# Performance work log

Measured on AMD Instinct MI355X. Metric: run time of the kernel, lower is better.

The kernel has to match this reference:

```python
import jax, jax.numpy as jnp
import numpy as np

# ---- grid / spectral configuration (matches init_kwargs) ----
_LONS_HALF = [20 + 4 * i for i in range(1, 97)]
LONS = _LONS_HALF + _LONS_HALF[::-1]          # 192 rings, pole to pole
NLAT = len(LONS)                               # 192
TRUNC = 191
M = TRUNC + 1                                  # zonal wavenumbers kept
MAX_NLON = max(LONS)                           # 404
SLON = np.concatenate([[0], np.cumsum(LONS)[:-1]]).astype(np.int64)
NGRID = int(np.sum(LONS))                      # 41088
BATCH, CHAN = 16, 64
TWO_PI = 2.0 * np.pi


def _legpoly(mmax, lmax, x):
    """(-1)^m c^l_m P^l_m(x), shape (mmax+1, lmax+1, len(x)); same recurrences as source."""
    nmax = max(mmax, lmax)
    vdm = np.zeros((nmax + 1, nmax + 1, len(x)), dtype=np.float64)
    norm_factor = np.sqrt(4 * np.pi)  # forward transform (inverse=False)
    vdm[0, 0, :] = norm_factor / np.sqrt(4 * np.pi)
    for n in range(1, nmax + 1):
        vdm[n - 1, n, :] = np.sqrt(2 * n + 1) * x * vdm[n - 1, n - 1, :]
        vdm[n, n, :] = np.sqrt((2 * n + 1) * (1 + x) * (1 - x) / 2 / n) * vdm[n - 1, n - 1, :]
    for n in range(2, nmax + 1):
        for m in range(0, n - 1):
            vdm[m, n, :] = (x * np.sqrt((2 * n - 1) / (n - m) * (2 * n + 1) / (n + m)) * vdm[m, n - 1, :]
                            - np.sqrt((n + m - 1) / (n - m) * (2 * n + 1) / (2 * n - 3) * (n - m - 1) / (n + m)) * vdm[m, n - 2, :])
    return vdm[:mmax + 1, :lmax + 1]


def _build_buffers():
    # Legendre-Gauss nodes/weights on [-1, 1]
    xlg, wlg = np.polynomial.legendre.leggauss(NLAT)
    theta = np.flip(np.arccos(xlg))
    pct = _legpoly(TRUNC, TRUNC, np.cos(theta))          # (M, L, K)
    weight = (pct * wlg[None, None, :]).astype(np.float32)

    # Ragged per-ring real DFT expressed as masked cos/sin bases (== rfft, norm='forward')
    p = np.arange(MAX_NLON)
    m = np.arange(M)
    nlon = np.asarray(LONS, dtype=np.float64)[:, None, None]       # (K,1,1)
    ang = TWO_PI * m[None, None, :] * p[None, :, None] / nlon      # (K,P,M)
    valid = (p[None, :, None] < nlon) & (m[None, None, :] <= (np.asarray(LONS)[:, None, None] // 2))
    cos_basis = np.where(valid, np.cos(ang) / nlon, 0.0).astype(np.float32)
    sin_basis = np.where(valid, -np.sin(ang) / nlon, 0.0).astype(np.float32)

    # gather map: ring_idx[k, p] = SLON[k] + min(p, nlon_k - 1)  (clipped; basis masks the tail)
    ring_idx = (SLON[:, None] + np.minimum(p[None, :], np.asarray(LONS)[:, None] - 1)).astype(np.int32)
    return weight, cos_basis, sin_basis, ring_idx


def setup_inputs() -> dict:
    key = jax.random.key(0)
    x = jax.random.normal(key, (BATCH, CHAN, NGRID), dtype=jnp.float32)
    weight, cos_basis, sin_basis, ring_idx = _build_buffers()
    return {
        "x": x,
        "weight": jnp.asarray(weight),
        "cos_basis": jnp.asarray(cos_basis),
        "sin_basis": jnp.asarray(sin_basis),
        "ring_idx": jnp.asarray(ring_idx),
    }


def reference(x, weight, cos_basis, sin_basis, ring_idx):
    # gather grid points into padded rings: [..., K, P]
    xr = x[..., ring_idx]
    # per-ring rfft (norm='forward'), restricted to m <= TRUNC, scaled by 2*pi
    re = TWO_PI * jnp.einsum("bckp,kpm->bckm", xr, cos_basis)
    im = TWO_PI * jnp.einsum("bckp,kpm->bckm", xr, sin_basis)
    # weighted Legendre contraction over latitudes k: [..., l, m]
    rl = jnp.einsum("bckm,mlk->bclm", re, weight)
    il = jnp.einsum("bckm,mlk->bclm", im, weight)
    # real/imag stacked (== torch.view_as_real of the complex output)
    return jnp.stack((rl, il), axis=-1)
```

## Files before the change

### kernel.cpp

```cpp
#include <hip/hip_runtime.h>

#define NLAT 192
#define MM   192
#define LL   192
#define PMAX 404
#define NGRID 41088
#define BC   1024
#define TWO_PI_F 6.2831853071795864769f

__device__ __forceinline__ int kmin_of_m(int m) {
    return (m <= 12) ? 0 : ((m - 11) >> 1);
}

__global__ __launch_bounds__(256) void sht_stage1(
    const float* __restrict__ x,
    const float* __restrict__ cosb,
    const float* __restrict__ sinb,
    const int*   __restrict__ ring,
    float* __restrict__ ws,
    int bc0, int bcc)
{
    const int k   = blockIdx.z;
    const int m0  = blockIdx.y * 64;
    const int bct = blockIdx.x * 64;
    const int tid = threadIdx.x;
    const int tx  = tid & 15;
    const int ty  = tid >> 4;

    const int slon = ring[k * PMAX];
    const int nlon = ring[k * PMAX + PMAX - 1] - slon + 1;

    float* __restrict__ re_ws = ws;
    float* __restrict__ im_ws = ws + (size_t)MM * NLAT * bcc;

    if (m0 > (nlon >> 1)) {
        const int klo16 = kmin_of_m(m0) & ~15;
        if (k < klo16 || k > (NLAT - 1) - klo16) return;
        const float4 z = {0.f, 0.f, 0.f, 0.f};
#pragma unroll
        for (int j = 0; j < 4; ++j) {
            const int m = m0 + 4 * ty + j;
            const size_t base = ((size_t)m * NLAT + k) * bcc + bct + 4 * tx;
            *(float4*)&re_ws[base] = z;
            *(float4*)&im_ws[base] = z;
        }
        return;
    }

    __shared__ float xs[16][68];
    __shared__ float cs[16][64];
    __shared__ float ss[16][64];

    float accr[4][4] = {{0.f}};
    float acci[4][4] = {{0.f}};

    for (int p0 = 0; p0 < nlon; p0 += 16) {
        {
            const int pq = (tid & 3) * 4;
            const int bl = tid >> 2;
            float4 v = {0.f, 0.f, 0.f, 0.f};
            if (p0 + pq < nlon)
                v = *(const float4*)(x + (size_t)(bc0 + bct + bl) * NGRID + slon + p0 + pq);
            xs[pq + 0][bl] = v.x;
            xs[pq + 1][bl] = v.y;
            xs[pq + 2][bl] = v.z;
            xs[pq + 3][bl] = v.w;
        }
        {
            const int mq = (tid & 15) * 4;
            const int pl = tid >> 4;
            float4 c = {0.f, 0.f, 0.f, 0.f};
            float4 s = {0.f, 0.f, 0.f, 0.f};
            if (p0 + pl < PMAX) {
                const size_t off = ((size_t)k * PMAX + p0 + pl) * MM + m0 + mq;
                c = *(const float4*)(cosb + off);
                s = *(const float4*)(sinb + off);
            }
            *(float4*)&cs[pl][mq] = c;
            *(float4*)&ss[pl][mq] = s;
        }
        __syncthreads();

#pragma unroll
        for (int pp = 0; pp < 16; ++pp) {
            float xv[4], cv[4], sv[4];
            *(float4*)xv = *(const float4*)&xs[pp][4 * tx];
            *(float4*)cv = *(const float4*)&cs[pp][4 * ty];
            *(float4*)sv = *(const float4*)&ss[pp][4 * ty];
#pragma unroll
            for (int i = 0; i < 4; ++i)
#pragma unroll
                for (int j = 0; j < 4; ++j) {
                    accr[i][j] += xv[i] * cv[j];
                    acci[i][j] += xv[i] * sv[j];
                }
        }
        __syncthreads();
    }

#pragma unroll
    for (int j = 0; j < 4; ++j) {
        const int m = m0 + 4 * ty + j;
        const size_t base = ((size_t)m * NLAT + k) * bcc + bct + 4 * tx;
        float4 r = {accr[0][j] * TWO_PI_F, accr[1][j] * TWO_PI_F,
                    accr[2][j] * TWO_PI_F, accr[3][j] * TWO_PI_F};
        float4 s = {acci[0][j] * TWO_PI_F, acci[1][j] * TWO_PI_F,
                    acci[2][j] * TWO_PI_F, acci[3][j] * TWO_PI_F};
        *(float4*)&re_ws[base] = r;
        *(float4*)&im_ws[base] = s;
    }
}

__global__ __launch_bounds__(256) void sht_stage2(
    const float* __restrict__ ws,
    float* __restrict__ ws2,
    const float* __restrict__ weight,
    int bcc)
{
    const int m   = blockIdx.z;
    const int l0  = blockIdx.y * 64;
    const int bct = blockIdx.x * 128;
    if (l0 + 63 < m) return;

    const int tid = threadIdx.x;
    const int tx  = tid & 15;
    const int ty  = tid >> 4;

    const int klo16 = kmin_of_m(m) & ~15;
    const int pcnt  = 96 - klo16;

    const float* __restrict__ re_ws = ws;
    const float* __restrict__ im_ws = ws + (size_t)MM * NLAT * bcc;

    __shared__ float Ar[16][128];
    __shared__ float Br[16][128];
    __shared__ float Ai[16][128];
    __shared__ float Bi[16][128];
    __shared__ float wl[16][68];

    float accr[8][4] = {{0.f}};
    float acci[8][4] = {{0.f}};

    const bool modd = (m & 1) != 0;
    const int  srow = tid >> 5;
    const int  scol = (tid & 31) * 4;
    const int  wkk  = tid & 15;
    const int  wlw  = tid >> 4;

    for (int pc = 0; pc < pcnt; pc += 16) {
        const int p0 = klo16 + pc;
#pragma unroll
        for (int pass = 0; pass < 2; ++pass) {
            const int row = srow + pass * 8;
            const size_t offa = ((size_t)m * NLAT + (p0 + row)) * bcc + bct + scol;
            const size_t offb = ((size_t)m * NLAT + (191 - p0 - row)) * bcc + bct + scol;
            const float4 ar = *(const float4*)&re_ws[offa];
            const float4 br = *(const float4*)&re_ws[offb];
            const float4 ai = *(const float4*)&im_ws[offa];
            const float4 bi = *(const float4*)&im_ws[offb];
            float4 er = {ar.x + br.x, ar.y + br.y, ar.z + br.z, ar.w + br.w};
            float4 od = {ar.x - br.x, ar.y - br.y, ar.z - br.z, ar.w - br.w};
            float4 ei = {ai.x + bi.x, ai.y + bi.y, ai.z + bi.z, ai.w + bi.w};
            float4 oi = {ai.x - bi.x, ai.y - bi.y, ai.z - bi.z, ai.w - bi.w};
            if (modd) { float4 t = er; er = od; od = t; t = ei; ei = oi; oi = t; }
            *(float4*)&Ar[row][scol] = er;
            *(float4*)&Br[row][scol] = od;
            *(float4*)&Ai[row][scol] = ei;
            *(float4*)&Bi[row][scol] = oi;
        }
        {
#pragma unroll
            for (int r = 0; r < 4; ++r) {
                const int lc = wlw + r * 16;
                wl[wkk][lc] = weight[((size_t)m * LL + l0 + lc) * NLAT + p0 + wkk];
            }
        }
        __syncthreads();

#pragma unroll
        for (int kk = 0; kk < 16; ++kk) {
            const float4 ea = *(const float4*)&Ar[kk][4 * tx];
            const float4 eb = *(const float4*)&Ar[kk][64 + 4 * tx];
            const float4 oa = *(const float4*)&Br[kk][4 * tx];
            const float4 ob = *(const float4*)&Br[kk][64 + 4 * tx];
            const float4 fa = *(const float4*)&Ai[kk][4 * tx];
            const float4 fb = *(const float4*)&Ai[kk][64 + 4 * tx];
            const float4 ga = *(const float4*)&Bi[kk][4 * tx];
            const float4 gb = *(const float4*)&Bi[kk][64 + 4 * tx];
            const float4 wv = *(const float4*)&wl[kk][4 * ty];
            const float er8[8] = {ea.x, ea.y, ea.z, ea.w, eb.x, eb.y, eb.z, eb.w};
            const float or8[8] = {oa.x, oa.y, oa.z, oa.w, ob.x, ob.y, ob.z, ob.w};
            const float ei8[8] = {fa.x, fa.y, fa.z, fa.w, fb.x, fb.y, fb.z, fb.w};
            const float oi8[8] = {ga.x, ga.y, ga.z, ga.w, gb.x, gb.y, gb.z, gb.w};
#pragma unroll
            for (int i = 0; i < 8; ++i) {
                accr[i][0] += er8[i] * wv.x;
                accr[i][1] += or8[i] * wv.y;
                accr[i][2] += er8[i] * wv.z;
                accr[i][3] += or8[i] * wv.w;
                acci[i][0] += ei8[i] * wv.x;
                acci[i][1] += oi8[i] * wv.y;
                acci[i][2] += ei8[i] * wv.z;
                acci[i][3] += oi8[i] * wv.w;
            }
        }
        __syncthreads();
    }

    float* __restrict__ re2 = ws2;
    float* __restrict__ im2 = ws2 + (size_t)MM * LL * bcc;
#pragma unroll
    for (int j = 0; j < 4; ++j) {
        const int l = l0 + 4 * ty + j;
        if (l < m) continue;
        const size_t base = ((size_t)m * LL + l) * bcc + bct;
        float4 r0 = {accr[0][j], accr[1][j], accr[2][j], accr[3][j]};
        float4 r1 = {accr[4][j], accr[5][j], accr[6][j], accr[7][j]};
        float4 i0 = {acci[0][j], acci[1][j], acci[2][j], acci[3][j]};
        float4 i1 = {acci[4][j], acci[5][j], acci[6][j], acci[7][j]};
        *(float4*)&re2[base + 4 * tx]      = r0;
        *(float4*)&re2[base + 64 + 4 * tx] = r1;
        *(float4*)&im2[base + 4 * tx]      = i0;
        *(float4*)&im2[base + 64 + 4 * tx] = i1;
    }
}

__global__ __launch_bounds__(256) void sht_transpose(
    const float* __restrict__ ws2,
    float* __restrict__ out,
    int bc0, int bcc)
{
    const int l   = blockIdx.z;
    const int m0  = blockIdx.y * 64;
    const int bct = blockIdx.x * 64;
    const int tid = threadIdx.x;

    __shared__ float t2r[64][66];
    __shared__ float t2i[64][66];

    const bool anynz = (m0 <= l);
    if (anynz) {
        const float* __restrict__ re2 = ws2;
        const float* __restrict__ im2 = ws2 + (size_t)MM * LL * bcc;
        const int bl4 = (tid & 15) * 4;
        const int mr  = tid >> 4;
#pragma unroll
        for (int r = 0; r < 4; ++r) {
            const int row = mr + r * 16;
            const size_t off = ((size_t)(m0 + row) * LL + l) * bcc + bct + bl4;
            const float4 a = *(const float4*)&re2[off];
            const float4 b = *(const float4*)&im2[off];
            t2r[bl4 + 0][row] = a.x; t2r[bl4 + 1][row] = a.y;
            t2r[bl4 + 2][row] = a.z; t2r[bl4 + 3][row] = a.w;
            t2i[bl4 + 0][row] = b.x; t2i[bl4 + 1][row] = b.y;
            t2i[bl4 + 2][row] = b.z; t2i[bl4 + 3][row] = b.w;
        }
    }
    __syncthreads();

    const int mq  = tid & 31;
    const int bcw = tid >> 5;
#pragma unroll
    for (int r = 0; r < 8; ++r) {
        const int bcl = bcw + 8 * r;
        const int bc  = bc0 + bct + bcl;
        const int m   = m0 + 2 * mq;
        float4 v = {0.f, 0.f, 0.f, 0.f};
        if (anynz) {
            const float2 rr = *(const float2*)&t2r[bcl][2 * mq];
            const float2 ii = *(const float2*)&t2i[bcl][2 * mq];
            if (m     <= l) { v.x = rr.x; v.y = ii.x; }
            if (m + 1 <= l) { v.z = rr.y; v.w = ii.y; }
        }
        const size_t o = (((size_t)bc * LL + l) * MM + m) * 2;
        *(float4*)&out[o] = v;
    }
}

extern "C" void kernel_launch(void* const* d_in, const int* in_sizes, int n_in,
                              void* d_out, int out_size, void* d_ws, size_t ws_size,
                              hipStream_t stream)
{
    const float* x      = (const float*)d_in[0];
    const float* weight = (const float*)d_in[1];
    const float* cosb   = (const float*)d_in[2];
    const float* sinb   = (const float*)d_in[3];
    const int*   ring   = (const int*)d_in[4];
    float* out = (float*)d_out;
    float* wsf = (float*)d_ws;

    const size_t per_bc = 4ull * MM * NLAT * sizeof(float);
    int chunk = BC;
    while ((size_t)chunk * per_bc > ws_size && chunk > 128) chunk >>= 1;

    for (int bc0 = 0; bc0 < BC; bc0 += chunk) {
        float* ws2 = wsf + 2ull * MM * NLAT * chunk;
        dim3 grid1(chunk / 64, 3, NLAT);
        hipLaunchKernelGGL(sht_stage1, grid1, dim3(256), 0, stream,
                           x, cosb, sinb, ring, wsf, bc0, chunk);
        dim3 grid2(chunk / 128, 3, MM);
        hipLaunchKernelGGL(sht_stage2, grid2, dim3(256), 0, stream,
                           wsf, ws2, weight, chunk);
        dim3 grid3(chunk / 64, 3, LL);
        hipLaunchKernelGGL(sht_transpose, grid3, dim3(256), 0, stream,
                           ws2, out, bc0, chunk);
    }
}
```

Measured before the change: 1.039 ms.

## Exploit DFT cos/sin symmetry to halve longitude loop in stage 1

Result: faster. 974.5 us (-6.2%).

```diff
diff --git a/kernel.cpp b/kernel.cpp
--- a/kernel.cpp
+++ b/kernel.cpp
@@ -29,11 +29,12 @@
 
     const int slon = ring[k * PMAX];
     const int nlon = ring[k * PMAX + PMAX - 1] - slon + 1;
+    const int n2   = nlon >> 1;
 
     float* __restrict__ re_ws = ws;
     float* __restrict__ im_ws = ws + (size_t)MM * NLAT * bcc;
 
-    if (m0 > (nlon >> 1)) {
+    if (m0 > n2) {
         const int klo16 = kmin_of_m(m0) & ~15;
         if (k < klo16 || k > (NLAT - 1) - klo16) return;
         const float4 z = {0.f, 0.f, 0.f, 0.f};
@@ -47,24 +48,37 @@
         return;
     }
 
-    __shared__ float xs[16][68];
+    __shared__ float xe[16][68];
+    __shared__ float xo[16][68];
     __shared__ float cs[16][64];
     __shared__ float ss[16][64];
 
     float accr[4][4] = {{0.f}};
     float acci[4][4] = {{0.f}};
 
-    for (int p0 = 0; p0 < nlon; p0 += 16) {
+    for (int p0 = 0; p0 <= n2; p0 += 16) {
         {
             const int pq = (tid & 3) * 4;
             const int bl = tid >> 2;
-            float4 v = {0.f, 0.f, 0.f, 0.f};
-            if (p0 + pq < nlon)
-                v = *(const float4*)(x + (size_t)(bc0 + bct + bl) * NGRID + slon + p0 + pq);
-            xs[pq + 0][bl] = v.x;
-            xs[pq + 1][bl] = v.y;
-            xs[pq + 2][bl] = v.z;
-            xs[pq + 3][bl] = v.w;
+            const float* xrow = x + (size_t)(bc0 + bct + bl) * NGRID + slon;
+            float f[4];
+            if (p0 + pq + 3 <= n2) {
+                const float4 v = *(const float4*)(xrow + p0 + pq);
+                f[0] = v.x; f[1] = v.y; f[2] = v.z; f[3] = v.w;
+            } else {
+#pragma unroll
+                for (int j = 0; j < 4; ++j) {
+                    const int p = p0 + pq + j;
+                    f[j] = (p <= n2) ? xrow[p] : 0.f;
+                }
+            }
+#pragma unroll
+            for (int j = 0; j < 4; ++j) {
+                const int p = p0 + pq + j;
+                const float b = (p >= 1 && p < n2) ? xrow[nlon - p] : 0.f;
+                xe[pq + j][bl] = f[j] + b;
+                xo[pq + j][bl] = f[j] - b;
+            }
         }
         {
             const int mq = (tid & 15) * 4;
@@ -83,16 +97,17 @@
 
 #pragma unroll
         for (int pp = 0; pp < 16; ++pp) {
-            float xv[4], cv[4], sv[4];
-            *(float4*)xv = *(const float4*)&xs[pp][4 * tx];
+            float ev[4], ov[4], cv[4], sv[4];
+            *(float4*)ev = *(const float4*)&xe[pp][4 * tx];
+            *(float4*)ov = *(const float4*)&xo[pp][4 * tx];
             *(float4*)cv = *(const float4*)&cs[pp][4 * ty];
             *(float4*)sv = *(const float4*)&ss[pp][4 * ty];
 #pragma unroll
             for (int i = 0; i < 4; ++i)
 #pragma unroll
                 for (int j = 0; j < 4; ++j) {
-                    accr[i][j] += xv[i] * cv[j];
-                    acci[i][j] += xv[i] * sv[j];
+                    accr[i][j] += ev[i] * cv[j];
+                    acci[i][j] += ov[i] * sv[j];
                 }
         }
         __syncthreads();
```
